# Kernel tuning notes

Measured on AMD Instinct MI355X. Metric: run time of the kernel, lower is better.

## Reference

```python
import jax, jax.numpy as jnp
import numpy as np

EPS = 1e-8
BETA = 0.25


def setup_inputs() -> dict:
    key = jax.random.key(0)
    k1, k2 = jax.random.split(key)
    x = jax.random.normal(k1, (1024, 128, 128), dtype=jnp.float32)
    # 4 residual levels, 256 codes each, dim 128
    codebooks = jax.random.normal(k2, (4, 256, 128), dtype=jnp.float32)
    return {"x": x, "codebooks": codebooks}


def reference(x, codebooks):
    B, T, D = x.shape
    n_levels = codebooks.shape[0]
    xf = x.reshape(-1, D)                      # [N, D]
    residual = xf
    x_q = jnp.zeros_like(xf)
    losses, idxs, scalars = [], [], []
    for i in range(n_levels):                  # small fixed loop over codebook levels
        e = codebooks[i]                       # [K, D]
        e_n = e / (jnp.linalg.norm(e, axis=-1, keepdims=True) + EPS)
        r_n = residual / (jnp.linalg.norm(residual, axis=-1, keepdims=True) + EPS)
        sim = r_n @ e_n.T                      # [N, K] cosine similarity
        idx = jnp.argmax(sim, axis=-1)         # [N]
        d = e_n[idx]                           # [N, D] quantized unit direction
        s = jnp.sum(residual * d, axis=-1)     # [N] projection scalar
        q = s[:, None] * d                     # [N, D] quantized residual
        # VQ-VAE loss: commitment (beta) + codebook term
        loss = (BETA * jnp.mean((jax.lax.stop_gradient(q) - residual) ** 2)
                + jnp.mean((q - jax.lax.stop_gradient(residual)) ** 2))
        # straight-through estimator
        q_st = residual + jax.lax.stop_gradient(q - residual)
        x_q = x_q + q_st
        residual = residual - q_st
        losses.append(loss)
        idxs.append(idx)
        scalars.append(s)
    mean_loss = jnp.mean(jnp.stack(losses))
    all_indices = jnp.stack(idxs, axis=-1).reshape(B, T, -1)
    all_scalars = jnp.stack(scalars, axis=-1).reshape(B, T, -1)
    return x_q.reshape(B, T, D), mean_loss, all_indices, all_scalars
```

## Files before the change

kernel.cpp:

```cpp
#include <hip/hip_runtime.h>
#include <math.h>

#define EPSF 1e-8f

constexpr int D_    = 128;
constexpr int NTOK  = 131072;
constexpr int NLVL  = 4;
constexpr int NCODE = 256;
constexpr int TPB   = 256;
constexpr int TOKB  = 64;
constexpr int STR   = 132;

__global__ __launch_bounds__(64) void normalize_cb(const float* __restrict__ cb,
                                                   float* __restrict__ out) {
  int row = blockIdx.x;
  int t   = threadIdx.x;
  float a = cb[row * D_ + t];
  float b = cb[row * D_ + t + 64];
  float ss = a * a + b * b;
#pragma unroll
  for (int m = 32; m >= 1; m >>= 1) ss += __shfl_xor(ss, m);
  float denom = sqrtf(ss) + EPSF;
  out[row * D_ + t]      = a / denom;
  out[row * D_ + t + 64] = b / denom;
}

__global__ __launch_bounds__(TPB) void rvq_main(const float* __restrict__ x,
                                                const float* __restrict__ en,
                                                float* __restrict__ out_xq,
                                                float* __restrict__ out_idx,
                                                float* __restrict__ out_s,
                                                double* __restrict__ lossacc_g) {
  __shared__ float r_lds[TOKB * STR];
  __shared__ float e_lds[64 * STR];
  __shared__ float red[4];

  const int t  = threadIdx.x;
  const int kg = t & 15;
  const int tg = t >> 4;
  const size_t n0 = (size_t)blockIdx.x * TOKB;

  const float4* __restrict__ x4 = (const float4*)(x + n0 * D_);
#pragma unroll
  for (int g = t; g < TOKB * D_ / 4; g += TPB) {
    float4 v = x4[g];
    *(float4*)&r_lds[(g >> 5) * STR + ((g & 31) << 2)] = v;
  }

  for (int lvl = 0; lvl < NLVL; ++lvl) {
    float best[4];
    int   bidx[4];
#pragma unroll
    for (int i = 0; i < 4; ++i) { best[i] = -3e38f; bidx[i] = 1 << 30; }

    for (int c = 0; c < 4; ++c) {
      __syncthreads();
      const float4* __restrict__ eg =
          (const float4*)(en + (size_t)(lvl * NCODE + c * 64) * D_);
#pragma unroll
      for (int g = t; g < 64 * D_ / 4; g += TPB) {
        float4 v = eg[g];
        *(float4*)&e_lds[(g >> 5) * STR + ((g & 31) << 2)] = v;
      }
      __syncthreads();

      float sim[4][4];
#pragma unroll
      for (int i = 0; i < 4; ++i)
#pragma unroll
        for (int j = 0; j < 4; ++j) sim[i][j] = 0.f;

      const float* rb = &r_lds[(tg * 4) * STR];
      const float* eb = &e_lds[kg * STR];
#pragma unroll 4
      for (int d = 0; d < D_; d += 4) {
        float4 rv[4];
#pragma unroll
        for (int i = 0; i < 4; ++i) rv[i] = *(const float4*)&rb[i * STR + d];
#pragma unroll
        for (int j = 0; j < 4; ++j) {
          float4 ev = *(const float4*)&eb[(j * 16) * STR + d];
#pragma unroll
          for (int i = 0; i < 4; ++i) {
            sim[i][j] += rv[i].x * ev.x;
            sim[i][j] += rv[i].y * ev.y;
            sim[i][j] += rv[i].z * ev.z;
            sim[i][j] += rv[i].w * ev.w;
          }
        }
      }

#pragma unroll
      for (int j = 0; j < 4; ++j) {
        int code = c * 64 + j * 16 + kg;
#pragma unroll
        for (int i = 0; i < 4; ++i) {
          float sv = sim[i][j];
          if (sv > best[i] || (sv == best[i] && code < bidx[i])) {
            best[i] = sv; bidx[i] = code;
          }
        }
      }
    }

#pragma unroll
    for (int m = 8; m >= 1; m >>= 1) {
#pragma unroll
      for (int i = 0; i < 4; ++i) {
        float ob = __shfl_xor(best[i], m);
        int   oi = __shfl_xor(bidx[i], m);
        if (ob > best[i] || (ob == best[i] && oi < bidx[i])) {
          best[i] = ob; bidx[i] = oi;
        }
      }
    }

    float lacc = 0.f;
#pragma unroll
    for (int i = 0; i < 4; ++i) {
      int row = tg * 4 + i;
      int idx = bidx[i];
      const float* ev = en + (size_t)(lvl * NCODE + idx) * D_ + kg * 8;
      float4 ea  = *(const float4*)ev;
      float4 eb2 = *(const float4*)(ev + 4);
      float* rp  = &r_lds[row * STR + kg * 8];
      float4 ra  = *(const float4*)rp;
      float4 rb2 = *(const float4*)(rp + 4);
      float sp = ra.x * ea.x + ra.y * ea.y + ra.z * ea.z + ra.w * ea.w +
                 rb2.x * eb2.x + rb2.y * eb2.y + rb2.z * eb2.z + rb2.w * eb2.w;
#pragma unroll
      for (int m = 8; m >= 1; m >>= 1) sp += __shfl_xor(sp, m);

      float4 na, nb;
      na.x = ra.x - sp * ea.x;   na.y = ra.y - sp * ea.y;
      na.z = ra.z - sp * ea.z;   na.w = ra.w - sp * ea.w;
      nb.x = rb2.x - sp * eb2.x; nb.y = rb2.y - sp * eb2.y;
      nb.z = rb2.z - sp * eb2.z; nb.w = rb2.w - sp * eb2.w;
      *(float4*)rp       = na;
      *(float4*)(rp + 4) = nb;
      lacc += na.x * na.x + na.y * na.y + na.z * na.z + na.w * na.w +
              nb.x * nb.x + nb.y * nb.y + nb.z * nb.z + nb.w * nb.w;

      if (kg == 0) {
        size_t n = n0 + row;
        out_idx[n * 4 + lvl] = (float)idx;
        out_s[n * 4 + lvl]   = sp;
      }
    }

#pragma unroll
    for (int m = 32; m >= 1; m >>= 1) lacc += __shfl_xor(lacc, m);
    if ((t & 63) == 0) red[t >> 6] = lacc;
    __syncthreads();
    if (t == 0)
      atomicAdd(&lossacc_g[lvl], (double)(red[0] + red[1] + red[2] + red[3]));
  }

  __syncthreads();
  float4* __restrict__ o4 = (float4*)(out_xq + n0 * D_);
#pragma unroll
  for (int g = t; g < TOKB * D_ / 4; g += TPB) {
    float4 xv = x4[g];
    float4 rv = *(const float4*)&r_lds[(g >> 5) * STR + ((g & 31) << 2)];
    float4 o;
    o.x = xv.x - rv.x; o.y = xv.y - rv.y; o.z = xv.z - rv.z; o.w = xv.w - rv.w;
    o4[g] = o;
  }
}

__global__ void finalize_loss(const double* __restrict__ lossacc_g,
                              float* __restrict__ out_loss) {
  double tot = lossacc_g[0] + lossacc_g[1] + lossacc_g[2] + lossacc_g[3];
  out_loss[0] = (float)(1.25 * tot / (4.0 * 16777216.0));
}

extern "C" void kernel_launch(void* const* d_in, const int* in_sizes, int n_in,
                              void* d_out, int out_size, void* d_ws, size_t ws_size,
                              hipStream_t stream) {
  const float* x  = (const float*)d_in[0];
  const float* cb = (const float*)d_in[1];

  float* out      = (float*)d_out;
  float* out_xq   = out;
  float* out_loss = out + (size_t)NTOK * D_;
  float* out_idx  = out_loss + 1;
  float* out_s    = out_idx + (size_t)NTOK * NLVL;

  double* lossacc = (double*)d_ws;
  float*  en      = (float*)((char*)d_ws + 256);

  hipMemsetAsync(d_ws, 0, 256, stream);
  normalize_cb<<<NLVL * NCODE, 64, 0, stream>>>(cb, en);
  rvq_main<<<NTOK / TOKB, TPB, 0, stream>>>(x, en, out_xq, out_idx, out_s, lossacc);
  finalize_loss<<<1, 1, 0, stream>>>(lossacc, out_loss);

  (void)in_sizes; (void)n_in; (void)out_size; (void)ws_size;
}
```

Before: 711.4 us.

## Keep each token's residual in registers and scan codebook via uniform global loads

Replaces the LDS-tiled 4x4 register-blocked similarity GEMM with a one-thread-per-token scheme: each thread holds its 128-float residual in registers and loops over all 256 codes, reading codebook entries through wave-uniform (scalar/broadcast) global loads. This removes the LDS staging of codebook chunks, the per-chunk barriers and the cross-lane argmax shuffles, and it takes s directly as the best similarity instead of recomputing the dot product. In exchange it needs about 128+ VGPRs per thread, which lowers occupancy, and it drops the explicit lowest-index tie-break in favour of strict greater-than. It also computes the similarity against the unnormalized residual, which gives the same argmax, and skips the residual norm.

```diff
diff --git a/kernel.cpp b/kernel.cpp
--- a/kernel.cpp
+++ b/kernel.cpp
@@ -7,8 +7,6 @@
 constexpr int NTOK  = 131072;
 constexpr int NLVL  = 4;
 constexpr int NCODE = 256;
-constexpr int TPB   = 256;
-constexpr int TOKB  = 64;
 constexpr int STR   = 132;
 
 __global__ __launch_bounds__(64) void normalize_cb(const float* __restrict__ cb,
@@ -25,146 +23,105 @@
   out[row * D_ + t + 64] = b / denom;
 }
 
-__global__ __launch_bounds__(TPB) void rvq_main(const float* __restrict__ x,
+__global__ __launch_bounds__(256) void rvq_main(const float* __restrict__ x,
                                                 const float* __restrict__ en,
                                                 float* __restrict__ out_xq,
                                                 float* __restrict__ out_idx,
                                                 float* __restrict__ out_s,
                                                 double* __restrict__ lossacc_g) {
-  __shared__ float r_lds[TOKB * STR];
-  __shared__ float e_lds[64 * STR];
-  __shared__ float red[4];
+  __shared__ float stage[64 * STR];
 
-  const int t  = threadIdx.x;
-  const int kg = t & 15;
-  const int tg = t >> 4;
-  const size_t n0 = (size_t)blockIdx.x * TOKB;
+  const int t    = threadIdx.x;
+  const int lane = t & 63;
+  const int w    = t >> 6;
+  const size_t tok0 = (size_t)blockIdx.x * 256;
+  const size_t myTok = tok0 + (size_t)w * 64 + lane;
 
-  const float4* __restrict__ x4 = (const float4*)(x + n0 * D_);
+  float r[128];
+
+  for (int w2 = 0; w2 < 4; ++w2) {
+    __syncthreads();
+    const float4* __restrict__ src = (const float4*)(x + (tok0 + (size_t)w2 * 64) * D_);
+    for (int g = t; g < 64 * 32; g += 256) {
+      float4 v = src[g];
+      *(float4*)&stage[(g >> 5) * STR + ((g & 31) << 2)] = v;
+    }
+    __syncthreads();
+    if (w == w2) {
 #pragma unroll
-  for (int g = t; g < TOKB * D_ / 4; g += TPB) {
-    float4 v = x4[g];
-    *(float4*)&r_lds[(g >> 5) * STR + ((g & 31) << 2)] = v;
+      for (int d4 = 0; d4 < 32; ++d4) {
+        float4 v = *(const float4*)&stage[lane * STR + d4 * 4];
+        r[d4 * 4 + 0] = v.x; r[d4 * 4 + 1] = v.y;
+        r[d4 * 4 + 2] = v.z; r[d4 * 4 + 3] = v.w;
+      }
+    }
   }
 
   for (int lvl = 0; lvl < NLVL; ++lvl) {
-    float best[4];
-    int   bidx[4];
+    const float* __restrict__ eL = en + (size_t)lvl * NCODE * D_;
+
+    float best = -3.0e38f;
+    int   bidx = 0;
+
+    for (int code = 0; code < NCODE; ++code) {
+      const float* __restrict__ ec = eL + code * D_;
+      float s0 = 0.f, s1 = 0.f, s2 = 0.f, s3 = 0.f;
 #pragma unroll
-    for (int i = 0; i < 4; ++i) { best[i] = -3e38f; bidx[i] = 1 << 30; }
+      for (int d = 0; d < D_; d += 4) {
+        s0 = fmaf(ec[d + 0], r[d + 0], s0);
+        s1 = fmaf(ec[d + 1], r[d + 1], s1);
+        s2 = fmaf(ec[d + 2], r[d + 2], s2);
+        s3 = fmaf(ec[d + 3], r[d + 3], s3);
+      }
+      float sv = (s0 + s1) + (s2 + s3);
+      if (sv > best) { best = sv; bidx = code; }
+    }
 
-    for (int c = 0; c < 4; ++c) {
-      __syncthreads();
-      const float4* __restrict__ eg =
-          (const float4*)(en + (size_t)(lvl * NCODE + c * 64) * D_);
+    float s = best;
+
+    const float* __restrict__ eW = eL + bidx * D_;
+    float l2 = 0.f;
 #pragma unroll
-      for (int g = t; g < 64 * D_ / 4; g += TPB) {
-        float4 v = eg[g];
-        *(float4*)&e_lds[(g >> 5) * STR + ((g & 31) << 2)] = v;
-      }
-      __syncthreads();
+    for (int d = 0; d < D_; d += 4) {
+      float4 ev = *(const float4*)&eW[d];
+      float n0 = r[d + 0] - s * ev.x;
+      float n1 = r[d + 1] - s * ev.y;
+      float n2 = r[d + 2] - s * ev.z;
+      float n3 = r[d + 3] - s * ev.w;
+      r[d + 0] = n0; r[d + 1] = n1; r[d + 2] = n2; r[d + 3] = n3;
+      l2 += n0 * n0 + n1 * n1 + n2 * n2 + n3 * n3;
+    }
 
-      float sim[4][4];
-#pragma unroll
-      for (int i = 0; i < 4; ++i)
-#pragma unroll
-        for (int j = 0; j < 4; ++j) sim[i][j] = 0.f;
-
-      const float* rb = &r_lds[(tg * 4) * STR];
-      const float* eb = &e_lds[kg * STR];
-#pragma unroll 4
-      for (int d = 0; d < D_; d += 4) {
-        float4 rv[4];
-#pragma unroll
-        for (int i = 0; i < 4; ++i) rv[i] = *(const float4*)&rb[i * STR + d];
-#pragma unroll
-        for (int j = 0; j < 4; ++j) {
-          float4 ev = *(const float4*)&eb[(j * 16) * STR + d];
-#pragma unroll
-          for (int i = 0; i < 4; ++i) {
-            sim[i][j] += rv[i].x * ev.x;
-            sim[i][j] += rv[i].y * ev.y;
-            sim[i][j] += rv[i].z * ev.z;
-            sim[i][j] += rv[i].w * ev.w;
-          }
-        }
-      }
+    out_idx[myTok * 4 + lvl] = (float)bidx;
+    out_s[myTok * 4 + lvl]   = s;
 
 #pragma unroll
-      for (int j = 0; j < 4; ++j) {
-        int code = c * 64 + j * 16 + kg;
+    for (int m = 32; m >= 1; m >>= 1) l2 += __shfl_xor(l2, m);
+    if (lane == 0) atomicAdd(&lossacc_g[lvl], (double)l2);
+  }
+
+  for (int w2 = 0; w2 < 4; ++w2) {
+    __syncthreads();
+    if (w == w2) {
 #pragma unroll
-        for (int i = 0; i < 4; ++i) {
-          float sv = sim[i][j];
-          if (sv > best[i] || (sv == best[i] && code < bidx[i])) {
-            best[i] = sv; bidx[i] = code;
-          }
-        }
+      for (int d4 = 0; d4 < 32; ++d4) {
+        float4 v;
+        v.x = r[d4 * 4 + 0]; v.y = r[d4 * 4 + 1];
+        v.z = r[d4 * 4 + 2]; v.w = r[d4 * 4 + 3];
+        *(float4*)&stage[lane * STR + d4 * 4] = v;
       }
     }
-
-#pragma unroll
-    for (int m = 8; m >= 1; m >>= 1) {
-#pragma unroll
-      for (int i = 0; i < 4; ++i) {
-        float ob = __shfl_xor(best[i], m);
-        int   oi = __shfl_xor(bidx[i], m);
-        if (ob > best[i] || (ob == best[i] && oi < bidx[i])) {
-          best[i] = ob; bidx[i] = oi;
-        }
-      }
+    __syncthreads();
+    const float4* __restrict__ xsrc = (const float4*)(x + (tok0 + (size_t)w2 * 64) * D_);
+    float4* __restrict__ odst = (float4*)(out_xq + (tok0 + (size_t)w2 * 64) * D_);
+    for (int g = t; g < 64 * 32; g += 256) {
+      float4 xv = xsrc[g];
+      float4 rv = *(const float4*)&stage[(g >> 5) * STR + ((g & 31) << 2)];
+      float4 o;
+      o.x = xv.x - rv.x; o.y = xv.y - rv.y;
+      o.z = xv.z - rv.z; o.w = xv.w - rv.w;
+      odst[g] = o;
     }
-
-    float lacc = 0.f;
-#pragma unroll
-    for (int i = 0; i < 4; ++i) {
-      int row = tg * 4 + i;
-      int idx = bidx[i];
-      const float* ev = en + (size_t)(lvl * NCODE + idx) * D_ + kg * 8;
-      float4 ea  = *(const float4*)ev;
-      float4 eb2 = *(const float4*)(ev + 4);
-      float* rp  = &r_lds[row * STR + kg * 8];
-      float4 ra  = *(const float4*)rp;
-      float4 rb2 = *(const float4*)(rp + 4);
-      float sp = ra.x * ea.x + ra.y * ea.y + ra.z * ea.z + ra.w * ea.w +
-                 rb2.x * eb2.x + rb2.y * eb2.y + rb2.z * eb2.z + rb2.w * eb2.w;
-#pragma unroll
-      for (int m = 8; m >= 1; m >>= 1) sp += __shfl_xor(sp, m);
-
-      float4 na, nb;
-      na.x = ra.x - sp * ea.x;   na.y = ra.y - sp * ea.y;
-      na.z = ra.z - sp * ea.z;   na.w = ra.w - sp * ea.w;
-      nb.x = rb2.x - sp * eb2.x; nb.y = rb2.y - sp * eb2.y;
-      nb.z = rb2.z - sp * eb2.z; nb.w = rb2.w - sp * eb2.w;
-      *(float4*)rp       = na;
-      *(float4*)(rp + 4) = nb;
-      lacc += na.x * na.x + na.y * na.y + na.z * na.z + na.w * na.w +
-              nb.x * nb.x + nb.y * nb.y + nb.z * nb.z + nb.w * nb.w;
-
-      if (kg == 0) {
-        size_t n = n0 + row;
-        out_idx[n * 4 + lvl] = (float)idx;
-        out_s[n * 4 + lvl]   = sp;
-      }
-    }
-
-#pragma unroll
-    for (int m = 32; m >= 1; m >>= 1) lacc += __shfl_xor(lacc, m);
-    if ((t & 63) == 0) red[t >> 6] = lacc;
-    __syncthreads();
-    if (t == 0)
-      atomicAdd(&lossacc_g[lvl], (double)(red[0] + red[1] + red[2] + red[3]));
-  }
-
-  __syncthreads();
-  float4* __restrict__ o4 = (float4*)(out_xq + n0 * D_);
-#pragma unroll
-  for (int g = t; g < TOKB * D_ / 4; g += TPB) {
-    float4 xv = x4[g];
-    float4 rv = *(const float4*)&r_lds[(g >> 5) * STR + ((g & 31) << 2)];
-    float4 o;
-    o.x = xv.x - rv.x; o.y = xv.y - rv.y; o.z = xv.z - rv.z; o.w = xv.w - rv.w;
-    o4[g] = o;
   }
 }
 
@@ -191,7 +148,7 @@
 
   hipMemsetAsync(d_ws, 0, 256, stream);
   normalize_cb<<<NLVL * NCODE, 64, 0, stream>>>(cb, en);
-  rvq_main<<<NTOK / TOKB, TPB, 0, stream>>>(x, en, out_xq, out_idx, out_s, lossacc);
+  rvq_main<<<NTOK / 256, 256, 0, stream>>>(x, en, out_xq, out_idx, out_s, lossacc);
   finalize_loss<<<1, 1, 0, stream>>>(lossacc, out_loss);
 
   (void)in_sizes; (void)n_in; (void)out_size; (void)ws_size;
```

Result: slower. 2.486 ms (+249.4%).
